# Performance work log

Hardware: AMD Instinct MI355X
Metric: run time of the kernel (lower is better)

## Reference

```python
import jax, jax.numpy as jnp
import numpy as np
from jax import lax

B, C, H, W = 4, 256, 64, 64
C8 = C // 8


def _conv1x1(x, w, b):
    # x: (B,C,H,W), w: (O,C) -> (B,O,H,W)
    return jnp.einsum('bchw,oc->bohw', x, w) + b[None, :, None, None]


def setup_inputs() -> dict:
    key = jax.random.key(0)
    ks = jax.random.split(key, 9)
    s1 = 1.0 / np.sqrt(C)          # fan-in scale for 1x1 convs
    sf = 1.0 / np.sqrt(2 * C * 9)  # fan-in scale for 3x3 conv
    return {
        'front_x':     jax.random.normal(ks[0], (B, C, H, W), jnp.float32),
        'cross_x':     jax.random.normal(ks[1], (B, C, H, W), jnp.float32),
        'front_x_hat': jax.random.normal(ks[2], (B, C, H, W), jnp.float32),
        'Wq': jax.random.normal(ks[3], (C8, C), jnp.float32) * s1,
        'bq': jnp.zeros((C8,), jnp.float32),
        'Wk': jax.random.normal(ks[4], (C8, C), jnp.float32) * s1,
        'bk': jnp.zeros((C8,), jnp.float32),
        'Wv': jax.random.normal(ks[5], (C, C), jnp.float32) * s1,
        'bv': jnp.zeros((C,), jnp.float32),
        'Wf': jax.random.normal(ks[6], (C, 2 * C, 3, 3), jnp.float32) * sf,
        'bf': jnp.zeros((C,), jnp.float32),
    }


def reference(front_x, cross_x, front_x_hat, Wq, bq, Wk, bk, Wv, bv, Wf, bf):
    b, c, h, w = front_x.shape
    hw = h * w
    # projections -> (B, C/8, HW)
    q = _conv1x1(cross_x, Wq, bq).reshape(b, -1, hw)
    k = _conv1x1(front_x, Wk, bk).reshape(b, -1, hw)
    # energy[b,i,j] = <key_i, query_j>  (B, HW, HW)
    energy = jnp.einsum('bci,bcj->bij', k, q)
    front_star = jnp.max(energy, axis=1)     # (B, HW) best key score per query
    front_arg = jnp.argmax(energy, axis=1)   # (B, HW) best key index per query
    # value projection and hard gather of best-matching value per position
    v = _conv1x1(front_x_hat, Wv, bv).reshape(b, c, hw)
    T = jnp.take_along_axis(v, front_arg[:, None, :], axis=2).reshape(b, c, h, w)
    S = front_star.reshape(b, 1, h, w)
    cat = jnp.concatenate([front_x, T], axis=1)  # (B, 2C, H, W)
    res = lax.conv_general_dilated(
        cat, Wf, window_strides=(1, 1), padding='SAME',
        dimension_numbers=('NCHW', 'OIHW', 'NCHW')) + bf[None, :, None, None]
    return front_x + res * S
```

## Files before the change

### kernel.cpp

```cpp
#include <hip/hip_runtime.h>

#define Bn 4
#define Cn 256
#define C8 32
#define Hn 64
#define Wn 64
#define HWn 4096
#define PADR 80
#define ROWS (HWn + 2 * PADR)
#define MARGIN 6e-3f

typedef __bf16 bf16x8 __attribute__((ext_vector_type(8)));
typedef float floatx4 __attribute__((ext_vector_type(4)));
typedef unsigned short u16x8 __attribute__((ext_vector_type(8)));

__device__ __forceinline__ unsigned short f2bf(float f) {
  union { float f; unsigned int u; } c; c.f = f;
  unsigned int u = c.u;
  return (unsigned short)((u + 0x7FFFu + ((u >> 16) & 1u)) >> 16);
}
__device__ __forceinline__ float bf2f(unsigned short h) {
  union { unsigned int u; float f; } c; c.u = ((unsigned int)h) << 16;
  return c.f;
}
__device__ __forceinline__ void gl_lds16(const void* g, void* l) {
  __builtin_amdgcn_global_load_lds(
      (__attribute__((address_space(1))) void*)(uintptr_t)g,
      (__attribute__((address_space(3))) void*)(uintptr_t)l, 16, 0, 0);
}

__global__ __launch_bounds__(1024) void proj_prep(
    const float* __restrict__ cross_x, const float* __restrict__ front_x,
    const float* __restrict__ Wq, const float* __restrict__ bq,
    const float* __restrict__ Wk, const float* __restrict__ bk,
    const float* __restrict__ Wv, const float* __restrict__ Wf,
    float* __restrict__ qf, float* __restrict__ kf,
    unsigned short* __restrict__ qhi, unsigned short* __restrict__ qlo,
    unsigned short* __restrict__ khi, unsigned short* __restrict__ klo,
    unsigned short* __restrict__ Wvb, unsigned short* __restrict__ Wfb,
    unsigned short* __restrict__ catF, unsigned short* __restrict__ zpad,
    int* __restrict__ cnt) {
  int bx = blockIdx.x;
  int tid = threadIdx.x;
  if (bx >= 512) {
    size_t t = (size_t)(bx - 512) * 1024 + tid;
    if (t == 0) cnt[0] = 0;
    if (t < 256) zpad[t] = 0;
    if (t < 163840) {
      int col = (int)(t & 255);
      int r4 = (int)(t >> 8);
      int bb = r4 / 160, rr = r4 % 160;
      int row = (rr < PADR) ? rr : (HWn + rr);
      catF[((size_t)bb * ROWS + row) * 256 + col] = 0;
    }
    if (t < 65536) Wvb[t] = f2bf(Wv[t]);
    {
      int tap = (int)(t / (256 * 512));
      int rem = (int)(t % (256 * 512));
      int o = rem / 512, ci = rem % 512;
      Wfb[t] = f2bf(Wf[((size_t)o * 512 + ci) * 9 + tap]);
    }
    return;
  }
  int lane = tid & 63, wv = tid >> 6;
  int slice = wv & 3;
  int chunk = wv >> 2;
  int jb = bx & 63;
  int b = (bx >> 6) & 3;
  int z = bx >> 8;
  int j = jb * 64 + lane;
  const float* x = (z == 0) ? cross_x : front_x;
  const float* Wraw = (z == 0) ? Wq : Wk;
  const float* bd = (z == 0) ? bq : bk;
  float* outp = (z == 0) ? qf : kf;
  unsigned short* hip_ = (z == 0) ? qhi : khi;
  unsigned short* lop_ = (z == 0) ? qlo : klo;
  int o0 = slice * 8;
  int c0 = chunk * 64;

  __shared__ __align__(16) float Wl[8192];
  __shared__ float part[3 * 4 * 8 * 64];

  for (int u = tid; u < 8192; u += 1024) {
    int c = u >> 5, o = u & 31;
    Wl[u] = Wraw[o * 256 + c];
  }
  __syncthreads();

  const float* xb = x + (size_t)b * Cn * HWn + j;
  floatx4 a0 = (floatx4)0.0f, a1 = (floatx4)0.0f;
#pragma unroll 16
  for (int c = c0; c < c0 + 64; ++c) {
    float xv = xb[(size_t)c * HWn];
    floatx4 wa = *reinterpret_cast<const floatx4*>(&Wl[c * 32 + o0]);
    floatx4 wb = *reinterpret_cast<const floatx4*>(&Wl[c * 32 + o0 + 4]);
    a0 += wa * xv;
    a1 += wb * xv;
  }
  if (chunk > 0) {
    float* dst = &part[(((chunk - 1) * 4 + slice) * 8) * 64];
#pragma unroll
    for (int o = 0; o < 4; ++o) { dst[o * 64 + lane] = a0[o]; dst[(o + 4) * 64 + lane] = a1[o]; }
  }
  __syncthreads();
  if (chunk != 0) return;
#pragma unroll
  for (int q = 0; q < 3; ++q) {
    const float* src = &part[((q * 4 + slice) * 8) * 64];
#pragma unroll
    for (int o = 0; o < 4; ++o) { a0[o] += src[o * 64 + lane]; a1[o] += src[(o + 4) * 64 + lane]; }
  }
  float acc[8];
#pragma unroll
  for (int o = 0; o < 4; ++o) { acc[o] = a0[o] + bd[o0 + o]; acc[o + 4] = a1[o] + bd[o0 + 4 + o]; }

  float* op = outp + ((size_t)b * HWn + j) * C8 + o0;
  u16x8 hv, lv;
#pragma unroll
  for (int o = 0; o < 8; ++o) {
    op[o] = acc[o];
    unsigned short h = f2bf(acc[o]);
    hv[o] = h;
    lv[o] = f2bf(acc[o] - bf2f(h));
  }
  *reinterpret_cast<u16x8*>(hip_ + ((size_t)b * HWn + j) * C8 + o0) = hv;
  *reinterpret_cast<u16x8*>(lop_ + ((size_t)b * HWn + j) * C8 + o0) = lv;
}

__global__ __launch_bounds__(1024, 8) void energy_cat(
    const unsigned short* __restrict__ khi, const unsigned short* __restrict__ klo,
    const unsigned short* __restrict__ qhi, const unsigned short* __restrict__ qlo,
    float* __restrict__ star, int* __restrict__ argb,
    int* __restrict__ cnt, int* __restrict__ list,
    const float* __restrict__ fx, const float* __restrict__ fxh,
    unsigned short* __restrict__ catF, unsigned short* __restrict__ xht) {
  int bx = blockIdx.x;
  if ((bx & 1) == 0) {
    int id = bx >> 1;
    int b = id >> 7;
    int j0 = (id & 127) * 32;
    int tid = threadIdx.x;
    int lane = tid & 63, wv = tid >> 6;
    int lm = lane & 15, lq = lane >> 4;

    __shared__ float bv1S[16][32];
    __shared__ int   bi1S[16][32];
    __shared__ float bv2S[16][32];

    bf16x8 qh[2], ql[2];
#pragma unroll
    for (int s = 0; s < 2; ++s) {
      int j = j0 + s * 16 + lm;
      qh[s] = *reinterpret_cast<const bf16x8*>(qhi + ((size_t)b * HWn + j) * 32 + lq * 8);
      ql[s] = *reinterpret_cast<const bf16x8*>(qlo + ((size_t)b * HWn + j) * 32 + lq * 8);
    }
    const unsigned short* kh_base = khi + (size_t)b * HWn * 32 + lq * 8;
    const unsigned short* kl_base = klo + (size_t)b * HWn * 32 + lq * 8;

    float b1[2], b2[2];
#pragma unroll
    for (int s = 0; s < 2; ++s) { b1[s] = -3.0e38f; b2[s] = -3.0e38f; }

    int ibase = wv * 256;
#pragma unroll 4
    for (int it = 0; it < 16; ++it) {
      int i0 = ibase + it * 16;
      bf16x8 ah = *reinterpret_cast<const bf16x8*>(kh_base + (size_t)(i0 + lm) * 32);
      bf16x8 al = *reinterpret_cast<const bf16x8*>(kl_base + (size_t)(i0 + lm) * 32);
#pragma unroll
      for (int s = 0; s < 2; ++s) {
        floatx4 acc = (floatx4)0.0f;
        acc = __builtin_amdgcn_mfma_f32_16x16x32_bf16(ah, qh[s], acc, 0, 0, 0);
        acc = __builtin_amdgcn_mfma_f32_16x16x32_bf16(ah, ql[s], acc, 0, 0, 0);
        acc = __builtin_amdgcn_mfma_f32_16x16x32_bf16(al, qh[s], acc, 0, 0, 0);
#pragma unroll
        for (int r = 0; r < 4; ++r) {
          unsigned code = (unsigned)(it * 4 + r);
          union { float f; unsigned u; } cv; cv.f = acc[r];
          cv.u = (cv.u & ~63u) | code;
          float vp = cv.f;
          b2[s] = __builtin_amdgcn_fmed3f(vp, b1[s], b2[s]);
          b1[s] = fmaxf(b1[s], vp);
        }
      }
    }
    int i1[2];
#pragma unroll
    for (int s = 0; s < 2; ++s) {
      union { float f; unsigned u; } cv; cv.f = b1[s];
      unsigned code = cv.u & 63u;
      i1[s] = ibase + (int)(code >> 2) * 16 + lq * 4 + (int)(code & 3u);
    }
#pragma unroll
    for (int s = 0; s < 2; ++s) {
#pragma unroll
      for (int m = 16; m <= 32; m <<= 1) {
        float ob1 = __shfl_xor(b1[s], m, 64);
        int oi1 = __shfl_xor(i1[s], m, 64);
        float ob2 = __shfl_xor(b2[s], m, 64);
        float c2;
        if (ob1 > b1[s] || (ob1 == b1[s] && oi1 < i1[s])) {
          c2 = fmaxf(b1[s], ob2);
          b1[s] = ob1; i1[s] = oi1;
        } else {
          c2 = fmaxf(ob1, b2[s]);
        }
        b2[s] = c2;
      }
      if (lq == 0) {
        bv1S[wv][s * 16 + lm] = b1[s];
        bi1S[wv][s * 16 + lm] = i1[s];
        bv2S[wv][s * 16 + lm] = b2[s];
      }
    }
    __syncthreads();
    if (tid < 32) {
      float B1 = bv1S[0][tid];
      int I1 = bi1S[0][tid];
      float B2 = bv2S[0][tid];
#pragma unroll
      for (int w = 1; w < 16; ++w) {
        float v1 = bv1S[w][tid];
        int ii = bi1S[w][tid];
        float v2 = bv2S[w][tid];
        if (v1 > B1) { B2 = fmaxf(B1, v2); B1 = v1; I1 = ii; }
        else B2 = fmaxf(B2, v1);
      }
      size_t o = (size_t)b * HWn + j0 + tid;
      union { float f; unsigned u; } cs; cs.f = B1;
      cs.u &= ~63u;
      star[o] = cs.f;
      argb[o] = I1;
      if (B1 - B2 < MARGIN) {
        int slot = atomicAdd(cnt, 1);
        list[slot] = (b << 12) | (j0 + (int)tid);
      }
    }
  } else {
    int id = bx >> 1;
    int j0 = (id & 63) * 64;
    int bz = id >> 6;
    int b = bz >> 1, which = bz & 1;
    int g4 = threadIdx.x >> 8;
    int tid = threadIdx.x & 255;
    int ci0 = g4 * 64;
    __shared__ unsigned short tile[4][64][66];

    const float* src = (which == 0) ? fx : fxh;
#pragma unroll
    for (int u = tid; u < 1024; u += 256) {
      int cl = u >> 4, h4 = (u & 15) * 4;
      floatx4 v = *reinterpret_cast<const floatx4*>(
          &src[((size_t)(b * Cn + ci0 + cl)) * HWn + j0 + h4]);
#pragma unroll
      for (int k = 0; k < 4; ++k) tile[g4][cl][h4 + k] = f2bf(v[k]);
    }
    __syncthreads();
#pragma unroll
    for (int u = tid; u < 512; u += 256) {
      int oct = u & 7, hw_l = u >> 3;
      u16x8 val;
#pragma unroll
      for (int k = 0; k < 8; ++k) val[k] = tile[g4][oct * 8 + k][hw_l];
      if (which == 0)
        *reinterpret_cast<u16x8*>(
            &catF[((size_t)b * ROWS + PADR + j0 + hw_l) * 256 + ci0 + oct * 8]) = val;
      else
        *reinterpret_cast<u16x8*>(
            &xht[((size_t)b * HWn + j0 + hw_l) * 256 + ci0 + oct * 8]) = val;
    }
  }
}

__global__ __launch_bounds__(256) void recheck_projv(
    const unsigned short* __restrict__ xht, const unsigned short* __restrict__ Wvb,
    const float* __restrict__ bv, unsigned short* __restrict__ vbf,
    const float* __restrict__ qf, const float* __restrict__ kf,
    const int* __restrict__ cnt, const int* __restrict__ list,
    float* __restrict__ star, int* __restrict__ argb) {
  int bx = blockIdx.x;
  if ((bx & 1) == 0) {
    int id = bx >> 1;
    int m0 = (id & 31) * 128;
    int o0 = ((id >> 5) & 1) * 128;
    int b = id >> 6;
    int tid = threadIdx.x;
    int lane = tid & 63, wv = tid >> 6;
    int wm = wv >> 1, wn = wv & 1;
    int lm = lane & 15, lq = lane >> 4;

    union SMu {
      struct { unsigned short A[2][128 * 32]; unsigned short B[2][128 * 32]; } st;
      unsigned short TS[128 * 136];
    };
    __shared__ __align__(16) SMu sm;

    floatx4 acc[4][4];
#pragma unroll
    for (int im = 0; im < 4; ++im)
#pragma unroll
      for (int in = 0; in < 4; ++in) acc[im][in] = (floatx4)0.0f;

    const int srow = lane >> 2;
    const int soff = (((lane & 3) ^ ((lane >> 3) & 3)) * 8);
    const int sa = (lq ^ ((lm >> 1) & 3)) * 8;
    const unsigned short* ag = Wvb + (size_t)o0 * 256;
    const unsigned short* bg = xht + ((size_t)b * HWn + m0) * 256;

    auto STAGE = [&](int buf, int kc) {
#pragma unroll
      for (int i = 0; i < 2; ++i) {
        int r0 = wv * 32 + i * 16;
        gl_lds16(ag + ((size_t)(r0 + srow)) * 256 + kc + soff, &sm.st.A[buf][r0 * 32]);
        gl_lds16(bg + ((size_t)(r0 + srow)) * 256 + kc + soff, &sm.st.B[buf][r0 * 32]);
      }
    };
    auto COMPUTE = [&](int buf) {
      bf16x8 afr[4];
#pragma unroll
      for (int im = 0; im < 4; ++im)
        afr[im] = *reinterpret_cast<const bf16x8*>(
            &sm.st.A[buf][(wm * 64 + im * 16 + lm) * 32 + sa]);
#pragma unroll
      for (int in = 0; in < 4; ++in) {
        bf16x8 bfr = *reinterpret_cast<const bf16x8*>(
            &sm.st.B[buf][(wn * 64 + in * 16 + lm) * 32 + sa]);
#pragma unroll
        for (int im = 0; im < 4; ++im)
          acc[im][in] = __builtin_amdgcn_mfma_f32_16x16x32_bf16(
              afr[im], bfr, acc[im][in], 0, 0, 0);
      }
    };

    STAGE(0, 0);
#pragma unroll 2
    for (int st = 0; st < 8; ++st) {
      __builtin_amdgcn_s_barrier();
      if (st < 7) {
        STAGE((st + 1) & 1, (st + 1) * 32);
        asm volatile("s_waitcnt vmcnt(4)" ::: "memory");
      } else {
        asm volatile("s_waitcnt vmcnt(0)" ::: "memory");
      }
      __builtin_amdgcn_s_barrier();
      __builtin_amdgcn_sched_barrier(0);
      COMPUTE(st & 1);
    }
    __builtin_amdgcn_s_barrier();

#pragma unroll
    for (int in = 0; in < 4; ++in) {
      int pl = wn * 64 + in * 16 + lm;
#pragma unroll
      for (int im = 0; im < 4; ++im) {
#pragma unroll
        for (int r = 0; r < 4; ++r) {
          int ol = wm * 64 + im * 16 + lq * 4 + r;
          sm.TS[pl * 136 + ol] = f2bf(acc[im][in][r] + bv[o0 + ol]);
        }
      }
    }
    __syncthreads();
    for (int idx = tid; idx < 128 * 16; idx += 256) {
      int p = idx >> 4, ch = idx & 15;
      u16x8 val = *reinterpret_cast<const u16x8*>(&sm.TS[p * 136 + ch * 8]);
      *reinterpret_cast<u16x8*>(
          &vbf[((size_t)b * HWn + m0 + p) * 256 + o0 + ch * 8]) = val;
    }
  } else {
    __shared__ double bvS[4];
    __shared__ int biS[4];
    int n = cnt[0];
    int tid = threadIdx.x;
    int lane = tid & 63, wv = tid >> 6;
    for (int idx = bx >> 1; idx < n; idx += 256) {
      int e = list[idx];
      int b = e >> 12, j = e & 4095;
      const float* qp = qf + ((size_t)b * HWn + j) * 32;
      double qj[32];
#pragma unroll
      for (int o = 0; o < 32; ++o) qj[o] = (double)qp[o];
      double best = -1.0e300;
      int bi = 1 << 30;
      for (int i = tid; i < HWn; i += 256) {
        const float* kp = kf + ((size_t)b * HWn + i) * 32;
        double s = 0.0;
#pragma unroll
        for (int o = 0; o < 32; ++o) s += (double)kp[o] * qj[o];
        if (s > best) { best = s; bi = i; }
      }
#pragma unroll
      for (int m = 1; m < 64; m <<= 1) {
        double ob = __shfl_xor(best, m, 64);
        int oi = __shfl_xor(bi, m, 64);
        if (ob > best || (ob == best && oi < bi)) { best = ob; bi = oi; }
      }
      if (lane == 0) { bvS[wv] = best; biS[wv] = bi; }
      __syncthreads();
      if (tid == 0) {
#pragma unroll
        for (int w = 1; w < 4; ++w) {
          if (bvS[w] > best || (bvS[w] == best && biS[w] < bi)) {
            best = bvS[w]; bi = biS[w];
          }
        }
        star[(size_t)b * HWn + j] = (float)best;
        argb[(size_t)b * HWn + j] = bi;
      }
      __syncthreads();
    }
  }
}

__global__ __launch_bounds__(256) void conv_mfma(
    const unsigned short* __restrict__ catF, const unsigned short* __restrict__ Wfb,
    const unsigned short* __restrict__ vbf, const int* __restrict__ argb,
    const unsigned short* __restrict__ zpad, unsigned short* __restrict__ Pg) {
  int m0 = blockIdx.x * 128;
  int o0 = blockIdx.y * 128;
  int bz = blockIdx.z;
  int b = bz / 3, g = bz % 3;
  int dy = g - 1;
  int tid = threadIdx.x;
  int lane = tid & 63;
  int wv = tid >> 6;
  int wm = wv >> 1, wn = wv & 1;
  int lm = lane & 15, lq = lane >> 4;
  const bool lane_first = (lm == 0);
  const bool lane_last = (lm == 15);

  __shared__ __align__(16) unsigned short AS[2][3 * 128 * 32];
  __shared__ __align__(16) unsigned short BS[2][144 * 32];

  floatx4 acc[4][4];
#pragma unroll
  for (int im = 0; im < 4; ++im)
#pragma unroll
    for (int in = 0; in < 4; ++in) acc[im][in] = (floatx4)0.0f;

  const int srow = lane >> 2;
  const int soff = (((lane & 3) ^ ((lane >> 3) & 3)) * 8);
  const int sa = (lq ^ ((lm >> 1) & 3)) * 8;
  const unsigned short* catb =
      catF + ((size_t)b * ROWS + PADR + m0 + dy * 64 - 1) * 256;
  const unsigned short* ag = Wfb + ((size_t)(g * 3) * 256 + o0) * 512;

  const unsigned short* tsrc[9];
#pragma unroll
  for (int s = 0; s < 9; ++s) tsrc[s] = zpad;
  if (wv == 3) {
    int p0 = m0 + dy * 64 - 1 + srow;
#pragma unroll
    for (int s = 0; s < 9; ++s) {
      int p = p0 + s * 16;
      bool v = ((unsigned)p < (unsigned)HWn);
      int aj = v ? argb[(size_t)b * HWn + (v ? p : 0)] : 0;
      tsrc[s] = v ? (vbf + ((size_t)b * HWn + aj) * 256) : zpad;
    }
  }

  auto STAGE = [&](unsigned short* ASb, unsigned short* BSb, int kc) {
    if (wv < 3) {
      const unsigned short* at = ag + (size_t)wv * 256 * 512;
#pragma unroll
      for (int s = 0; s < 8; ++s)
        gl_lds16(at + ((size_t)(s * 16 + srow)) * 512 + kc + soff,
                 &ASb[(wv * 128 + s * 16) * 32]);
    } else if (kc < 256) {
#pragma unroll
      for (int s = 0; s < 9; ++s)
        gl_lds16(catb + ((size_t)(s * 16 + srow)) * 256 + kc + soff,
                 &BSb[(s * 16) * 32]);
    } else {
      int kk = kc - 256;
#pragma unroll
      for (int s = 0; s < 9; ++s)
        gl_lds16(tsrc[s] + kk + soff, &BSb[(s * 16) * 32]);
    }
  };
  auto COMPUTE = [&](const unsigned short* ASb, const unsigned short* BSb) {
#pragma unroll
    for (int t = 0; t < 3; ++t) {
      bf16x8 afr[4];
#pragma unroll
      for (int im = 0; im < 4; ++im)
        afr[im] = *reinterpret_cast<const bf16x8*>(
            &ASb[(t * 128 + wm * 64 + im * 16 + lm) * 32 + sa]);
#pragma unroll
      for (int in = 0; in < 4; ++in) {
        int u = wn * 64 + in * 16 + lm + t;
        int sb = (lq ^ ((u >> 1) & 3)) * 8;
        u16x8 braw = *reinterpret_cast<const u16x8*>(&BSb[u * 32 + sb]);
        if ((t == 0 && in == 0 && lane_first) ||
            (t == 2 && in == 3 && lane_last))
          braw = (u16x8)(unsigned short)0;
        union { u16x8 u8; bf16x8 h; } cvt; cvt.u8 = braw;
#pragma unroll
        for (int im = 0; im < 4; ++im)
          acc[im][in] = __builtin_amdgcn_mfma_f32_16x16x32_bf16(
              afr[im], cvt.h, acc[im][in], 0, 0, 0);
      }
    }
  };

  STAGE(AS[0], BS[0], 0);
  __syncthreads();
  for (int kci = 0; kci < 16; kci += 2) {
    if (kci < 15) STAGE(AS[1], BS[1], (kci + 1) * 32);
    COMPUTE(AS[0], BS[0]);
    __syncthreads();
    if (kci < 14) STAGE(AS[0], BS[0], (kci + 2) * 32);
    COMPUTE(AS[1], BS[1]);
    __syncthreads();
  }

  unsigned short* P = Pg + ((size_t)(g * Bn + b) * Cn) * HWn;
#pragma unroll
  for (int in = 0; in < 4; ++in) {
    int p = m0 + wn * 64 + in * 16 + lm;
#pragma unroll
    for (int im = 0; im < 4; ++im) {
      int ob = o0 + wm * 64 + im * 16 + lq * 4;
#pragma unroll
      for (int r = 0; r < 4; ++r)
        P[(size_t)(ob + r) * HWn + p] = f2bf(acc[im][in][r]);
    }
  }
}

__global__ __launch_bounds__(256) void combine(
    const unsigned short* __restrict__ Pg, const float* __restrict__ fx,
    const float* __restrict__ bf, const float* __restrict__ star,
    float* __restrict__ out) {
  size_t e = ((size_t)blockIdx.x * 256 + threadIdx.x) * 8;
  int p = (int)(e & 4095);
  int bo = (int)(e >> 12);
  int o = bo & 255, b = bo >> 8;
  const size_t gs = (size_t)Bn * Cn * HWn;
  u16x8 q0 = *reinterpret_cast<const u16x8*>(Pg + e);
  u16x8 q1 = *reinterpret_cast<const u16x8*>(Pg + gs + e);
  u16x8 q2 = *reinterpret_cast<const u16x8*>(Pg + 2 * gs + e);
  float bias = bf[o];
  const float* sp = star + (size_t)b * HWn + p;
  const float* fp = fx + e;
  float* op = out + e;
#pragma unroll
  for (int h = 0; h < 2; ++h) {
    floatx4 s = *reinterpret_cast<const floatx4*>(sp + h * 4);
    floatx4 f = *reinterpret_cast<const floatx4*>(fp + h * 4);
    floatx4 r;
#pragma unroll
    for (int i = 0; i < 4; ++i) {
      int k = h * 4 + i;
      float a = bf2f(q0[k]) + bf2f(q1[k]) + bf2f(q2[k]);
      r[i] = f[i] + (a + bias) * s[i];
    }
    *reinterpret_cast<floatx4*>(op + h * 4) = r;
  }
}

extern "C" void kernel_launch(void* const* d_in, const int* in_sizes, int n_in,
                              void* d_out, int out_size, void* d_ws, size_t ws_size,
                              hipStream_t stream) {
  const float* front_x   = (const float*)d_in[0];
  const float* cross_x   = (const float*)d_in[1];
  const float* front_hat = (const float*)d_in[2];
  const float* Wq = (const float*)d_in[3];
  const float* bq = (const float*)d_in[4];
  const float* Wk = (const float*)d_in[5];
  const float* bk = (const float*)d_in[6];
  const float* Wv = (const float*)d_in[7];
  const float* bv = (const float*)d_in[8];
  const float* Wf = (const float*)d_in[9];
  const float* bf = (const float*)d_in[10];
  float* out = (float*)d_out;

  char* ws = (char*)d_ws;
  size_t off = 0;
  auto alloc = [&](size_t bytes) -> void* {
    void* p = (void*)(ws + off);
    off += (bytes + 255) & ~(size_t)255;
    return p;
  };
  unsigned short* Wvb = (unsigned short*)alloc(65536 * sizeof(unsigned short));
  unsigned short* Wfb = (unsigned short*)alloc((size_t)9 * 256 * 512 * sizeof(unsigned short));
  float* qf  = (float*)alloc((size_t)Bn * HWn * C8 * sizeof(float));
  float* kf  = (float*)alloc((size_t)Bn * HWn * C8 * sizeof(float));
  unsigned short* qhi = (unsigned short*)alloc((size_t)Bn * HWn * C8 * 2);
  unsigned short* qlo = (unsigned short*)alloc((size_t)Bn * HWn * C8 * 2);
  unsigned short* khi = (unsigned short*)alloc((size_t)Bn * HWn * C8 * 2);
  unsigned short* klo = (unsigned short*)alloc((size_t)Bn * HWn * C8 * 2);
  float*  star = (float*)alloc((size_t)Bn * HWn * sizeof(float));
  int*    argb = (int*)alloc((size_t)Bn * HWn * sizeof(int));
  int*    cnt  = (int*)alloc(256);
  int*    list = (int*)alloc((size_t)Bn * HWn * sizeof(int));
  unsigned short* xht = (unsigned short*)alloc((size_t)Bn * HWn * 256 * 2);
  unsigned short* vbf = (unsigned short*)alloc((size_t)Bn * HWn * 256 * 2);
  unsigned short* catF = (unsigned short*)alloc((size_t)Bn * ROWS * 256 * sizeof(unsigned short));
  unsigned short* zpad = (unsigned short*)alloc(256 * sizeof(unsigned short));
  unsigned short* Pg = (unsigned short*)alloc((size_t)3 * Bn * Cn * HWn * 2);

  proj_prep<<<dim3(512 + 1152), dim3(1024), 0, stream>>>(
      cross_x, front_x, Wq, bq, Wk, bk, Wv, Wf,
      qf, kf, qhi, qlo, khi, klo, Wvb, Wfb, catF, zpad, cnt);

  energy_cat<<<dim3(1024), dim3(1024), 0, stream>>>(
      khi, klo, qhi, qlo, star, argb, cnt, list,
      front_x, front_hat, catF, xht);

  recheck_projv<<<dim3(512), dim3(256), 0, stream>>>(
      xht, Wvb, bv, vbf, qf, kf, cnt, list, star, argb);

  conv_mfma<<<dim3(HWn / 128, Cn / 128, Bn * 3), dim3(256), 0, stream>>>(
      catF, Wfb, vbf, argb, zpad, Pg);

  combine<<<dim3((Bn * Cn * HWn / 8) / 256), dim3(256), 0, stream>>>(
      Pg, front_x, bf, star, out);
}
```

Measured before the change: 239.1 us.

## Move bf16 transpose into projection kernel and spread conv staging loads across waves

The front_x/front_hat bf16 transpose blocks move out of the energy kernel into the projection prep kernel, with their shared memory unioned with the projection buffers, so the energy kernel launches only argmax blocks. The conv kernel's staging no longer dedicates one wave to B-tile and gathered-T loads; all four waves now share the A and B loads, and each wave resolves only its own argb-gathered row pointers. The aim is better load balance in staging and an energy kernel that is purely MFMA work. The cost is higher LDS use and a heavier prep kernel.

```diff
diff --git a/kernel.cpp b/kernel.cpp
--- a/kernel.cpp
+++ b/kernel.cpp
@@ -29,8 +29,9 @@
       (__attribute__((address_space(3))) void*)(uintptr_t)l, 16, 0, 0);
 }
 
-__global__ __launch_bounds__(1024) void proj_prep(
+__global__ __launch_bounds__(1024) void proj_cat_prep(
     const float* __restrict__ cross_x, const float* __restrict__ front_x,
+    const float* __restrict__ front_hat,
     const float* __restrict__ Wq, const float* __restrict__ bq,
     const float* __restrict__ Wk, const float* __restrict__ bk,
     const float* __restrict__ Wv, const float* __restrict__ Wf,
@@ -38,12 +39,19 @@
     unsigned short* __restrict__ qhi, unsigned short* __restrict__ qlo,
     unsigned short* __restrict__ khi, unsigned short* __restrict__ klo,
     unsigned short* __restrict__ Wvb, unsigned short* __restrict__ Wfb,
-    unsigned short* __restrict__ catF, unsigned short* __restrict__ zpad,
-    int* __restrict__ cnt) {
+    unsigned short* __restrict__ catF, unsigned short* __restrict__ xht,
+    unsigned short* __restrict__ zpad, int* __restrict__ cnt) {
+  union SMu {
+    struct { float Wl[8192]; float part[3 * 4 * 8 * 64]; } pj;
+    unsigned short tile[4][64][66];
+  };
+  __shared__ __align__(16) SMu sm;
+
   int bx = blockIdx.x;
-  int tid = threadIdx.x;
-  if (bx >= 512) {
-    size_t t = (size_t)(bx - 512) * 1024 + tid;
+  int tid1k = threadIdx.x;
+
+  if (bx >= 1024) {
+    size_t t = (size_t)(bx - 1024) * 1024 + tid1k;
     if (t == 0) cnt[0] = 0;
     if (t < 256) zpad[t] = 0;
     if (t < 163840) {
@@ -62,12 +70,50 @@
     }
     return;
   }
+
+  if ((bx & 1) == 1) {
+    int id = bx >> 1;
+    int j0 = (id & 63) * 64;
+    int bz = id >> 6;
+    int b = bz >> 1, which = bz & 1;
+    int g4 = tid1k >> 8;
+    int tid = tid1k & 255;
+    int ci0 = g4 * 64;
+
+    const float* src = (which == 0) ? front_x : front_hat;
+#pragma unroll
+    for (int u = tid; u < 1024; u += 256) {
+      int cl = u >> 4, h4 = (u & 15) * 4;
+      floatx4 v = *reinterpret_cast<const floatx4*>(
+          &src[((size_t)(b * Cn + ci0 + cl)) * HWn + j0 + h4]);
+#pragma unroll
+      for (int k = 0; k < 4; ++k) sm.tile[g4][cl][h4 + k] = f2bf(v[k]);
+    }
+    __syncthreads();
+#pragma unroll
+    for (int u = tid; u < 512; u += 256) {
+      int oct = u & 7, hw_l = u >> 3;
+      u16x8 val;
+#pragma unroll
+      for (int k = 0; k < 8; ++k) val[k] = sm.tile[g4][oct * 8 + k][hw_l];
+      if (which == 0)
+        *reinterpret_cast<u16x8*>(
+            &catF[((size_t)b * ROWS + PADR + j0 + hw_l) * 256 + ci0 + oct * 8]) = val;
+      else
+        *reinterpret_cast<u16x8*>(
+            &xht[((size_t)b * HWn + j0 + hw_l) * 256 + ci0 + oct * 8]) = val;
+    }
+    return;
+  }
+
+  int id = bx >> 1;
+  int tid = tid1k;
   int lane = tid & 63, wv = tid >> 6;
   int slice = wv & 3;
   int chunk = wv >> 2;
-  int jb = bx & 63;
-  int b = (bx >> 6) & 3;
-  int z = bx >> 8;
+  int jb = id & 63;
+  int b = (id >> 6) & 3;
+  int z = id >> 8;
   int j = jb * 64 + lane;
   const float* x = (z == 0) ? cross_x : front_x;
   const float* Wraw = (z == 0) ? Wq : Wk;
@@ -78,8 +124,8 @@
   int o0 = slice * 8;
   int c0 = chunk * 64;
 
-  __shared__ __align__(16) float Wl[8192];
-  __shared__ float part[3 * 4 * 8 * 64];
+  float* Wl = sm.pj.Wl;
+  float* part = sm.pj.part;
 
   for (int u = tid; u < 8192; u += 1024) {
     int c = u >> 5, o = u & 31;
@@ -127,147 +173,108 @@
   *reinterpret_cast<u16x8*>(lop_ + ((size_t)b * HWn + j) * C8 + o0) = lv;
 }
 
-__global__ __launch_bounds__(1024, 8) void energy_cat(
+__global__ __launch_bounds__(1024) void energy_approx(
     const unsigned short* __restrict__ khi, const unsigned short* __restrict__ klo,
     const unsigned short* __restrict__ qhi, const unsigned short* __restrict__ qlo,
     float* __restrict__ star, int* __restrict__ argb,
-    int* __restrict__ cnt, int* __restrict__ list,
-    const float* __restrict__ fx, const float* __restrict__ fxh,
-    unsigned short* __restrict__ catF, unsigned short* __restrict__ xht) {
-  int bx = blockIdx.x;
-  if ((bx & 1) == 0) {
-    int id = bx >> 1;
-    int b = id >> 7;
-    int j0 = (id & 127) * 32;
-    int tid = threadIdx.x;
-    int lane = tid & 63, wv = tid >> 6;
-    int lm = lane & 15, lq = lane >> 4;
-
-    __shared__ float bv1S[16][32];
-    __shared__ int   bi1S[16][32];
-    __shared__ float bv2S[16][32];
-
-    bf16x8 qh[2], ql[2];
+    int* __restrict__ cnt, int* __restrict__ list) {
+  int b = blockIdx.y;
+  int j0 = blockIdx.x * 32;
+  int tid = threadIdx.x;
+  int lane = tid & 63, wv = tid >> 6;
+  int lm = lane & 15, lq = lane >> 4;
+
+  __shared__ float bv1S[16][32];
+  __shared__ int   bi1S[16][32];
+  __shared__ float bv2S[16][32];
+
+  bf16x8 qh[2], ql[2];
+#pragma unroll
+  for (int s = 0; s < 2; ++s) {
+    int j = j0 + s * 16 + lm;
+    qh[s] = *reinterpret_cast<const bf16x8*>(qhi + ((size_t)b * HWn + j) * 32 + lq * 8);
+    ql[s] = *reinterpret_cast<const bf16x8*>(qlo + ((size_t)b * HWn + j) * 32 + lq * 8);
+  }
+  const unsigned short* kh_base = khi + (size_t)b * HWn * 32 + lq * 8;
+  const unsigned short* kl_base = klo + (size_t)b * HWn * 32 + lq * 8;
+
+  float b1[2], b2[2];
+#pragma unroll
+  for (int s = 0; s < 2; ++s) { b1[s] = -3.0e38f; b2[s] = -3.0e38f; }
+
+  int ibase = wv * 256;
+#pragma unroll 4
+  for (int it = 0; it < 16; ++it) {
+    int i0 = ibase + it * 16;
+    bf16x8 ah = *reinterpret_cast<const bf16x8*>(kh_base + (size_t)(i0 + lm) * 32);
+    bf16x8 al = *reinterpret_cast<const bf16x8*>(kl_base + (size_t)(i0 + lm) * 32);
 #pragma unroll
     for (int s = 0; s < 2; ++s) {
-      int j = j0 + s * 16 + lm;
-      qh[s] = *reinterpret_cast<const bf16x8*>(qhi + ((size_t)b * HWn + j) * 32 + lq * 8);
-      ql[s] = *reinterpret_cast<const bf16x8*>(qlo + ((size_t)b * HWn + j) * 32 + lq * 8);
-    }
-    const unsigned short* kh_base = khi + (size_t)b * HWn * 32 + lq * 8;
-    const unsigned short* kl_base = klo + (size_t)b * HWn * 32 + lq * 8;
-
-    float b1[2], b2[2];
-#pragma unroll
-    for (int s = 0; s < 2; ++s) { b1[s] = -3.0e38f; b2[s] = -3.0e38f; }
-
-    int ibase = wv * 256;
-#pragma unroll 4
-    for (int it = 0; it < 16; ++it) {
-      int i0 = ibase + it * 16;
-      bf16x8 ah = *reinterpret_cast<const bf16x8*>(kh_base + (size_t)(i0 + lm) * 32);
-      bf16x8 al = *reinterpret_cast<const bf16x8*>(kl_base + (size_t)(i0 + lm) * 32);
-#pragma unroll
-      for (int s = 0; s < 2; ++s) {
-        floatx4 acc = (floatx4)0.0f;
-        acc = __builtin_amdgcn_mfma_f32_16x16x32_bf16(ah, qh[s], acc, 0, 0, 0);
-        acc = __builtin_amdgcn_mfma_f32_16x16x32_bf16(ah, ql[s], acc, 0, 0, 0);
-        acc = __builtin_amdgcn_mfma_f32_16x16x32_bf16(al, qh[s], acc, 0, 0, 0);
-#pragma unroll
-        for (int r = 0; r < 4; ++r) {
-          unsigned code = (unsigned)(it * 4 + r);
-          union { float f; unsigned u; } cv; cv.f = acc[r];
-          cv.u = (cv.u & ~63u) | code;
-          float vp = cv.f;
-          b2[s] = __builtin_amdgcn_fmed3f(vp, b1[s], b2[s]);
-          b1[s] = fmaxf(b1[s], vp);
-        }
-      }
-    }
-    int i1[2];
-#pragma unroll
-    for (int s = 0; s < 2; ++s) {
-      union { float f; unsigned u; } cv; cv.f = b1[s];
-      unsigned code = cv.u & 63u;
-      i1[s] = ibase + (int)(code >> 2) * 16 + lq * 4 + (int)(code & 3u);
-    }
-#pragma unroll
-    for (int s = 0; s < 2; ++s) {
-#pragma unroll
-      for (int m = 16; m <= 32; m <<= 1) {
-        float ob1 = __shfl_xor(b1[s], m, 64);
-        int oi1 = __shfl_xor(i1[s], m, 64);
-        float ob2 = __shfl_xor(b2[s], m, 64);
-        float c2;
-        if (ob1 > b1[s] || (ob1 == b1[s] && oi1 < i1[s])) {
-          c2 = fmaxf(b1[s], ob2);
-          b1[s] = ob1; i1[s] = oi1;
-        } else {
-          c2 = fmaxf(ob1, b2[s]);
-        }
-        b2[s] = c2;
-      }
-      if (lq == 0) {
-        bv1S[wv][s * 16 + lm] = b1[s];
-        bi1S[wv][s * 16 + lm] = i1[s];
-        bv2S[wv][s * 16 + lm] = b2[s];
-      }
-    }
-    __syncthreads();
-    if (tid < 32) {
-      float B1 = bv1S[0][tid];
-      int I1 = bi1S[0][tid];
-      float B2 = bv2S[0][tid];
-#pragma unroll
-      for (int w = 1; w < 16; ++w) {
-        float v1 = bv1S[w][tid];
-        int ii = bi1S[w][tid];
-        float v2 = bv2S[w][tid];
-        if (v1 > B1) { B2 = fmaxf(B1, v2); B1 = v1; I1 = ii; }
-        else B2 = fmaxf(B2, v1);
-      }
-      size_t o = (size_t)b * HWn + j0 + tid;
-      union { float f; unsigned u; } cs; cs.f = B1;
-      cs.u &= ~63u;
-      star[o] = cs.f;
-      argb[o] = I1;
-      if (B1 - B2 < MARGIN) {
-        int slot = atomicAdd(cnt, 1);
-        list[slot] = (b << 12) | (j0 + (int)tid);
-      }
-    }
-  } else {
-    int id = bx >> 1;
-    int j0 = (id & 63) * 64;
-    int bz = id >> 6;
-    int b = bz >> 1, which = bz & 1;
-    int g4 = threadIdx.x >> 8;
-    int tid = threadIdx.x & 255;
-    int ci0 = g4 * 64;
-    __shared__ unsigned short tile[4][64][66];
-
-    const float* src = (which == 0) ? fx : fxh;
-#pragma unroll
-    for (int u = tid; u < 1024; u += 256) {
-      int cl = u >> 4, h4 = (u & 15) * 4;
-      floatx4 v = *reinterpret_cast<const floatx4*>(
-          &src[((size_t)(b * Cn + ci0 + cl)) * HWn + j0 + h4]);
-#pragma unroll
-      for (int k = 0; k < 4; ++k) tile[g4][cl][h4 + k] = f2bf(v[k]);
-    }
-    __syncthreads();
-#pragma unroll
-    for (int u = tid; u < 512; u += 256) {
-      int oct = u & 7, hw_l = u >> 3;
-      u16x8 val;
-#pragma unroll
-      for (int k = 0; k < 8; ++k) val[k] = tile[g4][oct * 8 + k][hw_l];
-      if (which == 0)
-        *reinterpret_cast<u16x8*>(
-            &catF[((size_t)b * ROWS + PADR + j0 + hw_l) * 256 + ci0 + oct * 8]) = val;
-      else
-        *reinterpret_cast<u16x8*>(
-            &xht[((size_t)b * HWn + j0 + hw_l) * 256 + ci0 + oct * 8]) = val;
+      floatx4 acc = (floatx4)0.0f;
+      acc = __builtin_amdgcn_mfma_f32_16x16x32_bf16(ah, qh[s], acc, 0, 0, 0);
+      acc = __builtin_amdgcn_mfma_f32_16x16x32_bf16(ah, ql[s], acc, 0, 0, 0);
+      acc = __builtin_amdgcn_mfma_f32_16x16x32_bf16(al, qh[s], acc, 0, 0, 0);
+#pragma unroll
+      for (int r = 0; r < 4; ++r) {
+        unsigned code = (unsigned)(it * 4 + r);
+        union { float f; unsigned u; } cv; cv.f = acc[r];
+        cv.u = (cv.u & ~63u) | code;
+        float vp = cv.f;
+        b2[s] = __builtin_amdgcn_fmed3f(vp, b1[s], b2[s]);
+        b1[s] = fmaxf(b1[s], vp);
+      }
+    }
+  }
+  int i1[2];
+#pragma unroll
+  for (int s = 0; s < 2; ++s) {
+    union { float f; unsigned u; } cv; cv.f = b1[s];
+    unsigned code = cv.u & 63u;
+    i1[s] = ibase + (int)(code >> 2) * 16 + lq * 4 + (int)(code & 3u);
+  }
+#pragma unroll
+  for (int s = 0; s < 2; ++s) {
+#pragma unroll
+    for (int m = 16; m <= 32; m <<= 1) {
+      float ob1 = __shfl_xor(b1[s], m, 64);
+      int oi1 = __shfl_xor(i1[s], m, 64);
+      float ob2 = __shfl_xor(b2[s], m, 64);
+      float c2;
+      if (ob1 > b1[s] || (ob1 == b1[s] && oi1 < i1[s])) {
+        c2 = fmaxf(b1[s], ob2);
+        b1[s] = ob1; i1[s] = oi1;
+      } else {
+        c2 = fmaxf(ob1, b2[s]);
+      }
+      b2[s] = c2;
+    }
+    if (lq == 0) {
+      bv1S[wv][s * 16 + lm] = b1[s];
+      bi1S[wv][s * 16 + lm] = i1[s];
+      bv2S[wv][s * 16 + lm] = b2[s];
+    }
+  }
+  __syncthreads();
+  if (tid < 32) {
+    float B1 = bv1S[0][tid];
+    int I1 = bi1S[0][tid];
+    float B2 = bv2S[0][tid];
+#pragma unroll
+    for (int w = 1; w < 16; ++w) {
+      float v1 = bv1S[w][tid];
+      int ii = bi1S[w][tid];
+      float v2 = bv2S[w][tid];
+      if (v1 > B1) { B2 = fmaxf(B1, v2); B1 = v1; I1 = ii; }
+      else B2 = fmaxf(B2, v1);
+    }
+    size_t o = (size_t)b * HWn + j0 + tid;
+    union { float f; unsigned u; } cs; cs.f = B1;
+    cs.u &= ~63u;
+    star[o] = cs.f;
+    argb[o] = I1;
+    if (B1 - B2 < MARGIN) {
+      int slot = atomicAdd(cnt, 1);
+      list[slot] = (b << 12) | (j0 + (int)tid);
     }
   }
 }
@@ -445,37 +452,39 @@
       catF + ((size_t)b * ROWS + PADR + m0 + dy * 64 - 1) * 256;
   const unsigned short* ag = Wfb + ((size_t)(g * 3) * 256 + o0) * 512;
 
-  const unsigned short* tsrc[9];
-#pragma unroll
-  for (int s = 0; s < 9; ++s) tsrc[s] = zpad;
-  if (wv == 3) {
-    int p0 = m0 + dy * 64 - 1 + srow;
-#pragma unroll
-    for (int s = 0; s < 9; ++s) {
-      int p = p0 + s * 16;
-      bool v = ((unsigned)p < (unsigned)HWn);
-      int aj = v ? argb[(size_t)b * HWn + (v ? p : 0)] : 0;
-      tsrc[s] = v ? (vbf + ((size_t)b * HWn + aj) * 256) : zpad;
-    }
-  }
+  auto mk_tsrc = [&](int s) -> const unsigned short* {
+    int p = m0 + dy * 64 - 1 + s * 16 + srow;
+    bool v = ((unsigned)p < (unsigned)HWn);
+    int aj = argb[(size_t)b * HWn + (v ? p : 0)];
+    return v ? (vbf + ((size_t)b * HWn + aj) * 256) : zpad;
+  };
+  const unsigned short* tP0 = mk_tsrc(wv);
+  const unsigned short* tP1 = mk_tsrc(wv + 4);
+  const unsigned short* tP2 = (wv == 0) ? mk_tsrc(8) : zpad;
+  const int s0 = wv, s1 = wv + 4;
 
   auto STAGE = [&](unsigned short* ASb, unsigned short* BSb, int kc) {
-    if (wv < 3) {
-      const unsigned short* at = ag + (size_t)wv * 256 * 512;
-#pragma unroll
-      for (int s = 0; s < 8; ++s)
-        gl_lds16(at + ((size_t)(s * 16 + srow)) * 512 + kc + soff,
-                 &ASb[(wv * 128 + s * 16) * 32]);
-    } else if (kc < 256) {
-#pragma unroll
-      for (int s = 0; s < 9; ++s)
-        gl_lds16(catb + ((size_t)(s * 16 + srow)) * 256 + kc + soff,
-                 &BSb[(s * 16) * 32]);
+#pragma unroll
+    for (int i = 0; i < 6; ++i) {
+      int l = wv + i * 4;
+      int t = l >> 3, s = l & 7;
+      gl_lds16(ag + ((size_t)(t * 256 + s * 16 + srow)) * 512 + kc + soff,
+               &ASb[(t * 128 + s * 16) * 32]);
+    }
+    if (kc < 256) {
+      gl_lds16(catb + ((size_t)(s0 * 16 + srow)) * 256 + kc + soff,
+               &BSb[(s0 * 16) * 32]);
+      gl_lds16(catb + ((size_t)(s1 * 16 + srow)) * 256 + kc + soff,
+               &BSb[(s1 * 16) * 32]);
+      if (wv == 0)
+        gl_lds16(catb + ((size_t)(8 * 16 + srow)) * 256 + kc + soff,
+                 &BSb[(8 * 16) * 32]);
     } else {
       int kk = kc - 256;
-#pragma unroll
-      for (int s = 0; s < 9; ++s)
-        gl_lds16(tsrc[s] + kk + soff, &BSb[(s * 16) * 32]);
+      gl_lds16(tP0 + kk + soff, &BSb[(s0 * 16) * 32]);
+      gl_lds16(tP1 + kk + soff, &BSb[(s1 * 16) * 32]);
+      if (wv == 0)
+        gl_lds16(tP2 + kk + soff, &BSb[(8 * 16) * 32]);
     }
   };
   auto COMPUTE = [&](const unsigned short* ASb, const unsigned short* BSb) {
@@ -600,13 +609,12 @@
   unsigned short* zpad = (unsigned short*)alloc(256 * sizeof(unsigned short));
   unsigned short* Pg = (unsigned short*)alloc((size_t)3 * Bn * Cn * HWn * 2);
 
-  proj_prep<<<dim3(512 + 1152), dim3(1024), 0, stream>>>(
-      cross_x, front_x, Wq, bq, Wk, bk, Wv, Wf,
-      qf, kf, qhi, qlo, khi, klo, Wvb, Wfb, catF, zpad, cnt);
-
-  energy_cat<<<dim3(1024), dim3(1024), 0, stream>>>(
-      khi, klo, qhi, qlo, star, argb, cnt, list,
-      front_x, front_hat, catF, xht);
+  proj_cat_prep<<<dim3(1024 + 1152), dim3(1024), 0, stream>>>(
+      cross_x, front_x, front_hat, Wq, bq, Wk, bk, Wv, Wf,
+      qf, kf, qhi, qlo, khi, klo, Wvb, Wfb, catF, xht, zpad, cnt);
+
+  energy_approx<<<dim3(HWn / 32, Bn), dim3(1024), 0, stream>>>(
+      khi, klo, qhi, qlo, star, argb, cnt, list);
 
   recheck_projv<<<dim3(512), dim3(256), 0, stream>>>(
       xht, Wvb, bv, vbf, qf, kf, cnt, list, star, argb);
```

Result: no change. 237.0 us (-0.9%).
